# Kernel tuning notes

Hardware: AMD Instinct MI355X
Metric: run time of the kernel (lower is better)

Reference implementation:

```python
import jax, jax.numpy as jnp
import numpy as np

N = 100000   # nodes
E = 3200000  # directed edges
EPS = 1e-5   # batchnorm eps


def setup_inputs() -> dict:
    key = jax.random.key(0)
    ks = jax.random.split(key, 12)
    x = jax.random.normal(ks[0], (N, 128), jnp.float32)
    edge_index = jax.random.randint(ks[1], (2, E), 0, N, dtype=jnp.int32).astype(jnp.int64)
    W1 = jax.random.normal(ks[2], (128, 256), jnp.float32) * (1.0 / np.sqrt(128))
    W2 = jax.random.normal(ks[3], (256, 256), jnp.float32) * (1.0 / np.sqrt(256))
    W3 = jax.random.normal(ks[4], (256, 40), jnp.float32) * (1.0 / np.sqrt(256))
    return {
        "x": x, "edge_index": edge_index,
        "W1": W1, "b1": jnp.zeros((256,), jnp.float32),
        "W2": W2, "b2": jnp.zeros((256,), jnp.float32),
        "W3": W3, "b3": jnp.zeros((40,), jnp.float32),
        "g1": jnp.ones((256,), jnp.float32), "be1": jnp.zeros((256,), jnp.float32),
        "g2": jnp.ones((256,), jnp.float32), "be2": jnp.zeros((256,), jnp.float32),
    }


def _gcn_conv(x, src, dst, norm, W, b):
    # GCNConv: transform then normalized sparse aggregation (A_hat @ (x W)) + b
    h = x @ W                              # [N, F_out]
    msg = h[src] * norm[:, None]           # gather + edge scaling, [E+N, F_out]
    return jax.ops.segment_sum(msg, dst, num_segments=N) + b


def _bn(h, g, b):
    # BatchNorm over the node dimension (batch stats, biased variance)
    m = h.mean(axis=0)
    v = h.var(axis=0)
    return (h - m) * jax.lax.rsqrt(v + EPS) * g + b


def reference(x, edge_index, W1, b1, W2, b2, W3, b3, g1, be1, g2, be2):
    # add self-loops (A + I), symmetric degree normalization D^-1/2 (A+I) D^-1/2
    loop = jnp.arange(N, dtype=edge_index.dtype)
    src = jnp.concatenate([edge_index[0], loop])
    dst = jnp.concatenate([edge_index[1], loop])
    deg = jax.ops.segment_sum(jnp.ones_like(src, jnp.float32), dst, num_segments=N)
    dinv = jax.lax.rsqrt(jnp.maximum(deg, 1.0))
    norm = dinv[src] * dinv[dst]           # [E+N]

    h = _gcn_conv(x, src, dst, norm, W1, b1)
    h = jax.nn.relu(_bn(h, g1, be1))       # dropout: identity (eval mode)
    h = _gcn_conv(h, src, dst, norm, W2, b2)
    h = jax.nn.relu(_bn(h, g2, be2))
    h = _gcn_conv(h, src, dst, norm, W3, b3)
    return jax.nn.log_softmax(h, axis=1)
```

## Files before the change

### kernel.cpp

```cpp
#include <hip/hip_runtime.h>
#include <hip/hip_bf16.h>
#include <math.h>

#define NNODES 100000
#define NEDGES 3200000
#define BN_EPS 1e-5f
#define NCH 391

typedef unsigned int uint;
typedef unsigned short ushort;
typedef __attribute__((ext_vector_type(8))) short bf16x8;
typedef __attribute__((ext_vector_type(4))) float f32x4;

__device__ inline float bflo(uint u) { return __uint_as_float(u << 16); }
__device__ inline float bfhi(uint u) { return __uint_as_float(u & 0xffff0000u); }
__device__ inline ushort f2bf(float f) {
    __hip_bfloat16 h = __float2bfloat16(f);
    union { __hip_bfloat16 b; ushort u; } c; c.b = h; return c.u;
}


__global__ void k_hist(const int* __restrict__ dst, int* __restrict__ cnt) {
    int e = blockIdx.x * 256 + threadIdx.x;
    if (e < NEDGES) atomicAdd(&cnt[dst[e]], 1);
}

__global__ void k_deg(const int* __restrict__ cnt, float* __restrict__ dinv,
                      int* __restrict__ chunksums) {
    __shared__ int s[256];
    int i = blockIdx.x * 256 + threadIdx.x;
    int c = (i < NNODES) ? cnt[i] : 0;
    if (i < NNODES) dinv[i] = rsqrtf((float)c + 1.0f);
    s[threadIdx.x] = c;
    __syncthreads();
    for (int o = 128; o > 0; o >>= 1) {
        if (threadIdx.x < o) s[threadIdx.x] += s[threadIdx.x + o];
        __syncthreads();
    }
    if (threadIdx.x == 0) chunksums[blockIdx.x] = s[0];
}

__global__ void k_scan1(int* __restrict__ chunksums, int* __restrict__ rowstart) {
    __shared__ int s[512];
    int t = threadIdx.x;
    int v = (t < NCH) ? chunksums[t] : 0;
    s[t] = v;
    __syncthreads();
    for (int o = 1; o < 512; o <<= 1) {
        int add = (t >= o) ? s[t - o] : 0;
        __syncthreads();
        s[t] += add;
        __syncthreads();
    }
    if (t < NCH) chunksums[t] = s[t] - v;
    if (t == NCH - 1) rowstart[NNODES] = s[t];
}

__global__ void k_scan2(const int* __restrict__ cnt, const int* __restrict__ chunkbase,
                        int* __restrict__ rowstart, int* __restrict__ cursor) {
    __shared__ int s[256];
    int t = threadIdx.x;
    int i = blockIdx.x * 256 + t;
    int v = (i < NNODES) ? cnt[i] : 0;
    s[t] = v;
    __syncthreads();
    for (int o = 1; o < 256; o <<= 1) {
        int add = (t >= o) ? s[t - o] : 0;
        __syncthreads();
        s[t] += add;
        __syncthreads();
    }
    if (i < NNODES) {
        int excl = s[t] - v + chunkbase[blockIdx.x];
        rowstart[i] = excl;
        cursor[i]   = excl;
    }
}

__global__ void k_scatter(const int* __restrict__ src, const int* __restrict__ dst,
                          const float* __restrict__ dinv, int* __restrict__ cursor,
                          int2* __restrict__ pairs) {
    int e = blockIdx.x * 256 + threadIdx.x;
    if (e >= NEDGES) return;
    int s = src[e], d = dst[e];
    int p = atomicAdd(&cursor[d], 1);
    float w = dinv[s] * dinv[d];
    pairs[p] = make_int2(s, __float_as_int(w));
}


template <int F, bool BF16OUT>
__global__ __launch_bounds__(256) void k_aggb(
    const ushort* __restrict__ X, void* __restrict__ Yv,
    const int2* __restrict__ pairs, const int* __restrict__ rowstart,
    const float* __restrict__ dinv, const float* __restrict__ bias) {
    constexpr int VEC = F / 64;
    constexpr int NU  = VEC / 2;
    const int sub = threadIdx.x >> 6;
    const int t   = threadIdx.x & 63;
    const int d   = blockIdx.x * 4 + sub;
    if (d >= NNODES) return;
    const int r0 = rowstart[d], r1 = rowstart[d + 1];
    const size_t cb = (size_t)VEC * t;
    float acc[VEC] = {};
    int p = r0;
    for (; p + 8 <= r1; p += 8) {
        int2 e[8];
#pragma unroll
        for (int j = 0; j < 8; ++j) e[j] = pairs[p + j];
        if constexpr (NU == 2) {
            uint2 u[8];
#pragma unroll
            for (int j = 0; j < 8; ++j) u[j] = *(const uint2*)(X + (size_t)e[j].x * F + cb);
#pragma unroll
            for (int j = 0; j < 8; ++j) {
                float w = __int_as_float(e[j].y);
                acc[0]=fmaf(w,bflo(u[j].x),acc[0]); acc[1]=fmaf(w,bfhi(u[j].x),acc[1]);
                acc[2]=fmaf(w,bflo(u[j].y),acc[2]); acc[3]=fmaf(w,bfhi(u[j].y),acc[3]);
            }
        } else {
            uint u[8];
#pragma unroll
            for (int j = 0; j < 8; ++j) u[j] = *(const uint*)(X + (size_t)e[j].x * F + cb);
#pragma unroll
            for (int j = 0; j < 8; ++j) {
                float w = __int_as_float(e[j].y);
                acc[0]=fmaf(w,bflo(u[j]),acc[0]); acc[1]=fmaf(w,bfhi(u[j]),acc[1]);
            }
        }
    }
    for (; p < r1; ++p) {
        int2 e = pairs[p];
        float w = __int_as_float(e.y);
        if constexpr (NU == 2) {
            uint2 u = *(const uint2*)(X + (size_t)e.x * F + cb);
            acc[0]=fmaf(w,bflo(u.x),acc[0]); acc[1]=fmaf(w,bfhi(u.x),acc[1]);
            acc[2]=fmaf(w,bflo(u.y),acc[2]); acc[3]=fmaf(w,bfhi(u.y),acc[3]);
        } else {
            uint u = *(const uint*)(X + (size_t)e.x * F + cb);
            acc[0]=fmaf(w,bflo(u),acc[0]); acc[1]=fmaf(w,bfhi(u),acc[1]);
        }
    }
    float di = dinv[d], ws = di * di;
    if constexpr (NU == 2) {
        uint2 u = *(const uint2*)(X + (size_t)d * F + cb);
        acc[0]=fmaf(ws,bflo(u.x),acc[0]); acc[1]=fmaf(ws,bfhi(u.x),acc[1]);
        acc[2]=fmaf(ws,bflo(u.y),acc[2]); acc[3]=fmaf(ws,bfhi(u.y),acc[3]);
    } else {
        uint u = *(const uint*)(X + (size_t)d * F + cb);
        acc[0]=fmaf(ws,bflo(u),acc[0]); acc[1]=fmaf(ws,bfhi(u),acc[1]);
    }
    if (bias) {
#pragma unroll
        for (int j = 0; j < VEC; ++j) acc[j] += bias[cb + j];
    }
    if constexpr (BF16OUT) {
        uint* Y = (uint*)Yv;
        uint o0 = (uint)f2bf(acc[0]) | ((uint)f2bf(acc[1]) << 16);
        if constexpr (NU == 2) {
            uint o1 = (uint)f2bf(acc[2]) | ((uint)f2bf(acc[3]) << 16);
            *(uint2*)(Y + (size_t)d * (F/2) + cb/2) = make_uint2(o0, o1);
        } else {
            Y[(size_t)d * (F/2) + cb/2] = o0;
        }
    } else {
        float* Y = (float*)Yv;
        if constexpr (NU == 2) {
            float4 o; o.x=acc[0]; o.y=acc[1]; o.z=acc[2]; o.w=acc[3];
            *(float4*)(Y + (size_t)d * F + cb) = o;
        } else {
            *(float2*)(Y + (size_t)d * F + cb) = make_float2(acc[0], acc[1]);
        }
    }
}


__global__ __launch_bounds__(256) void k_agg40lsm(
    const ushort* __restrict__ X, float* __restrict__ out,
    const int2* __restrict__ pairs, const int* __restrict__ rowstart,
    const float* __restrict__ dinv, const float* __restrict__ bias) {
    int t = threadIdx.x;
    int wid = t >> 6, lane = t & 63;
    int sub = lane >> 5, l32 = lane & 31;
    int d = blockIdx.x * 8 + wid * 2 + sub;
    bool act = l32 < 20;
    int col = act ? 2 * l32 : 0;
    const int r0 = rowstart[d], r1 = rowstart[d + 1];
    float a0 = 0.f, a1 = 0.f;
    int p = r0;
    for (; p + 4 <= r1; p += 4) {
        int2 e0 = pairs[p], e1 = pairs[p+1], e2 = pairs[p+2], e3 = pairs[p+3];
        uint u0 = *(const uint*)(X + (size_t)e0.x * 40 + col);
        uint u1 = *(const uint*)(X + (size_t)e1.x * 40 + col);
        uint u2 = *(const uint*)(X + (size_t)e2.x * 40 + col);
        uint u3 = *(const uint*)(X + (size_t)e3.x * 40 + col);
        float w0 = __int_as_float(e0.y), w1 = __int_as_float(e1.y);
        float w2 = __int_as_float(e2.y), w3 = __int_as_float(e3.y);
        a0=fmaf(w0,bflo(u0),a0); a1=fmaf(w0,bfhi(u0),a1);
        a0=fmaf(w1,bflo(u1),a0); a1=fmaf(w1,bfhi(u1),a1);
        a0=fmaf(w2,bflo(u2),a0); a1=fmaf(w2,bfhi(u2),a1);
        a0=fmaf(w3,bflo(u3),a0); a1=fmaf(w3,bfhi(u3),a1);
    }
    for (; p < r1; ++p) {
        int2 e = pairs[p];
        uint u = *(const uint*)(X + (size_t)e.x * 40 + col);
        float w_ = __int_as_float(e.y);
        a0=fmaf(w_,bflo(u),a0); a1=fmaf(w_,bfhi(u),a1);
    }
    float di = dinv[d], ws = di * di;
    uint us = *(const uint*)(X + (size_t)d * 40 + col);
    a0=fmaf(ws,bflo(us),a0); a1=fmaf(ws,bfhi(us),a1);
    if (act) { a0 += bias[col]; a1 += bias[col + 1]; }
    else     { a0 = -INFINITY;  a1 = -INFINITY; }
    float mx = fmaxf(a0, a1);
    for (int o = 16; o > 0; o >>= 1) mx = fmaxf(mx, __shfl_xor(mx, o, 32));
    float e = act ? (expf(a0 - mx) + expf(a1 - mx)) : 0.f;
    float s = e;
    for (int o = 16; o > 0; o >>= 1) s += __shfl_xor(s, o, 32);
    float ls = logf(s);
    if (act)
        *(float2*)(out + (size_t)d * 40 + col) = make_float2(a0 - mx - ls, a1 - mx - ls);
}


__global__ void k_xtobf16(const float* __restrict__ X, ushort* __restrict__ O) {
    int i = blockIdx.x * 256 + threadIdx.x;
    float4 v = ((const float4*)X)[i];
    ushort4 o; o.x=f2bf(v.x); o.y=f2bf(v.y); o.z=f2bf(v.z); o.w=f2bf(v.w);
    ((ushort4*)O)[i] = o;
}

__global__ void k_wconv(const float* __restrict__ W, ushort* __restrict__ Wt, int K) {
    int n = blockIdx.x;
    for (int k = threadIdx.x; k < K; k += 256)
        Wt[n * K + k] = f2bf(W[(size_t)k * 256 + n]);
}


__device__ inline bf16x8 bnrelu8(bf16x8 v, const float* __restrict__ scsh, int ch) {
    bf16x8 r;
#pragma unroll
    for (int j = 0; j < 8; ++j) {
        float f = __uint_as_float(((uint)(ushort)v[j]) << 16);
        f = fmaxf(fmaf(f, scsh[ch + j], scsh[256 + ch + j]), 0.f);
        r[j] = (short)f2bf(f);
    }
    return r;
}

template <int K, bool BNA>
__global__ __launch_bounds__(256) void k_gmm(
    const ushort* __restrict__ A, const ushort* __restrict__ Bt,
    const float* __restrict__ scsh, ushort* __restrict__ C) {
    __shared__ ushort As[128 * 32];
    __shared__ ushort Bs[128 * 32];
    const int m0 = blockIdx.x * 128;
    const int n0 = blockIdx.y * 128;
    const int tid = threadIdx.x;
    const int lane = tid & 63;
    const int wid = tid >> 6;
    const int wr = wid >> 1, wc = wid & 1;
    const int sr1 = tid >> 2, sc = tid & 3;
    const int sr2 = sr1 + 64;
    const int ssl1 = sr1 * 32 + ((sc ^ ((sr1 >> 1) & 3)) * 8);
    const int ssl2 = sr2 * 32 + ((sc ^ ((sr2 >> 1) & 3)) * 8);
    const size_t ga1 = (size_t)min(m0 + sr1, NNODES - 1) * K + sc * 8;
    const size_t ga2 = (size_t)min(m0 + sr2, NNODES - 1) * K + sc * 8;
    const size_t gb1 = (size_t)(n0 + sr1) * K + sc * 8;
    const size_t gb2 = (size_t)(n0 + sr2) * K + sc * 8;
    const int kc = lane >> 4, rr = lane & 15;
    f32x4 acc[4][4] = {};
    for (int k0 = 0; k0 < K; k0 += 32) {
        bf16x8 av1 = *(const bf16x8*)(A + ga1 + k0);
        bf16x8 av2 = *(const bf16x8*)(A + ga2 + k0);
        bf16x8 bv1 = *(const bf16x8*)(Bt + gb1 + k0);
        bf16x8 bv2 = *(const bf16x8*)(Bt + gb2 + k0);
        if constexpr (BNA) {
            int ch = k0 + sc * 8;
            av1 = bnrelu8(av1, scsh, ch);
            av2 = bnrelu8(av2, scsh, ch);
        }
        if (k0) __syncthreads();
        *(bf16x8*)(As + ssl1) = av1;
        *(bf16x8*)(As + ssl2) = av2;
        *(bf16x8*)(Bs + ssl1) = bv1;
        *(bf16x8*)(Bs + ssl2) = bv2;
        __syncthreads();
        bf16x8 af[4], bfr[4];
#pragma unroll
        for (int f = 0; f < 4; ++f) {
            int ar = wr * 64 + f * 16 + rr;
            int br = wc * 64 + f * 16 + rr;
            af[f]  = *(const bf16x8*)(As + ar * 32 + ((kc ^ ((ar >> 1) & 3)) * 8));
            bfr[f] = *(const bf16x8*)(Bs + br * 32 + ((kc ^ ((br >> 1) & 3)) * 8));
        }
#pragma unroll
        for (int fm = 0; fm < 4; ++fm)
#pragma unroll
            for (int fn = 0; fn < 4; ++fn)
                acc[fm][fn] = __builtin_amdgcn_mfma_f32_16x16x32_bf16(af[fm], bfr[fn], acc[fm][fn], 0, 0, 0);
    }
    const int crow0 = m0 + wr * 64 + (lane >> 4) * 4;
    const int ccol0 = n0 + wc * 64 + (lane & 15);
#pragma unroll
    for (int fm = 0; fm < 4; ++fm) {
#pragma unroll
        for (int r = 0; r < 4; ++r) {
            int m = crow0 + fm * 16 + r;
            if (m >= NNODES) continue;
#pragma unroll
            for (int fn = 0; fn < 4; ++fn)
                C[(size_t)m * 256 + ccol0 + fn * 16] = f2bf(acc[fm][fn][r]);
        }
    }
}

__global__ void k_gemm3(const uint* __restrict__ A, const float* __restrict__ scsh,
                        const float* __restrict__ W, ushort* __restrict__ C) {
    __shared__ float aS[4][256];
    int m0 = blockIdx.x * 4;
    int t = threadIdx.x;
    for (int j = t; j < 512; j += 256) {
        int r = j >> 7, kk = j & 127;
        uint u = A[(size_t)(m0 + r) * 128 + kk];
        aS[r][2*kk]   = fmaxf(fmaf(bflo(u), scsh[2*kk],   scsh[256+2*kk]),   0.f);
        aS[r][2*kk+1] = fmaxf(fmaf(bfhi(u), scsh[2*kk+1], scsh[256+2*kk+1]), 0.f);
    }
    __syncthreads();
    int w = t >> 6, lane = t & 63;
    if (lane >= 40) return;
    float acc0 = 0.f, acc1 = 0.f;
#pragma unroll 8
    for (int k = 0; k < 256; k += 2) {
        acc0 = fmaf(aS[w][k],     W[k * 40 + lane],       acc0);
        acc1 = fmaf(aS[w][k + 1], W[(k + 1) * 40 + lane], acc1);
    }
    C[(size_t)(m0 + w) * 40 + lane] = f2bf(acc0 + acc1);
}


__global__ void k_bnstats_bf(const uint* __restrict__ H, float* __restrict__ sums) {
    int t = threadIdx.x;
    int pp = t & 127, half = t >> 7;
    size_t row0 = (size_t)blockIdx.x * 256 + half * 128;
    float s0=0, s20=0, s1=0, s21=0;
    for (int i = 0; i < 128; ++i) {
        size_t m = row0 + i;
        if (m >= NNODES) break;
        uint u = H[m * 128 + pp];
        float v0 = bflo(u), v1 = bfhi(u);
        s0 += v0; s20 += v0*v0; s1 += v1; s21 += v1*v1;
    }
    atomicAdd(&sums[2*pp],       s0);
    atomicAdd(&sums[2*pp+1],     s1);
    atomicAdd(&sums[256+2*pp],   s20);
    atomicAdd(&sums[256+2*pp+1], s21);
}

__global__ void k_bnfin(const float* __restrict__ sums, const float* __restrict__ g,
                        const float* __restrict__ be, float* __restrict__ scsh) {
    int c = threadIdx.x;
    float mean = sums[c] * (1.0f / NNODES);
    float var  = sums[256 + c] * (1.0f / NNODES) - mean * mean;
    float sc = g[c] * rsqrtf(var + BN_EPS);
    scsh[c] = sc;
    scsh[256 + c] = be[c] - mean * sc;
}


extern "C" void kernel_launch(void* const* d_in, const int* in_sizes, int n_in,
                              void* d_out, int out_size, void* d_ws, size_t ws_size,
                              hipStream_t stream) {
    const float* x  = (const float*)d_in[0];
    const int*   ei = (const int*)d_in[1];
    const float* W1 = (const float*)d_in[2];
    const float* W2 = (const float*)d_in[4];
    const float* W3 = (const float*)d_in[6];
    const float* b3 = (const float*)d_in[7];
    const float* g1 = (const float*)d_in[8];
    const float* be1 = (const float*)d_in[9];
    const float* g2 = (const float*)d_in[10];
    const float* be2 = (const float*)d_in[11];
    float* out = (float*)d_out;

    const int* esrc = ei;
    const int* edst = ei + NEDGES;

    char* p = (char*)d_ws;
    auto alloc = [&](size_t bytes) { char* r = p; p += (bytes + 511) & ~(size_t)511; return r; };
    float* dinv     = (float*)alloc((size_t)NNODES * 4);
    int*   cnt      = (int*)  alloc((size_t)NNODES * 4);
    int*   rowstart = (int*)  alloc((size_t)(NNODES + 1) * 4);
    int*   cursor   = (int*)  alloc((size_t)NNODES * 4);
    int*   chunksums= (int*)  alloc((size_t)NCH * 4);
    float* stats    = (float*)alloc((size_t)2048 * 4);
    ushort* W1t     = (ushort*)alloc((size_t)256 * 128 * 2);
    ushort* W2t     = (ushort*)alloc((size_t)256 * 256 * 2);
    int2*  pairs    = (int2*) alloc((size_t)NEDGES * 8);
    char*  R1       = alloc((size_t)NNODES * 256 * 2);
    char*  R2       = alloc((size_t)NNODES * 256 * 2);
    char*  R3       = alloc((size_t)NNODES * 256 * 2);

    ushort* xbf16 = (ushort*)R1;
    ushort* P_bf  = (ushort*)R1 + (size_t)NNODES * 128;
    ushort* t3_bf = (ushort*)R1;
    ushort* h1_bf = (ushort*)R2;
    ushort* h2_bf = (ushort*)R2;
    ushort* t_bf  = (ushort*)R3;

    float* sums1 = stats;        float* scsh1 = stats + 512;
    float* sums2 = stats + 1024; float* scsh2 = stats + 1536;

    hipMemsetAsync(cnt, 0, (size_t)NNODES * 4, stream);
    hipMemsetAsync(stats, 0, (size_t)2048 * 4, stream);

    const int EB = NEDGES / 256;
    const int NB = NCH;

    k_hist<<<EB, 256, 0, stream>>>(edst, cnt);
    k_deg<<<NB, 256, 0, stream>>>(cnt, dinv, chunksums);
    k_scan1<<<1, 512, 0, stream>>>(chunksums, rowstart);
    k_scan2<<<NB, 256, 0, stream>>>(cnt, chunksums, rowstart, cursor);
    k_scatter<<<EB, 256, 0, stream>>>(esrc, edst, dinv, cursor, pairs);

    k_wconv<<<256, 256, 0, stream>>>(W1, W1t, 128);
    k_wconv<<<256, 256, 0, stream>>>(W2, W2t, 256);
    k_xtobf16<<<NNODES * 128 / 4 / 256, 256, 0, stream>>>(x, xbf16);

    dim3 ggrid((NNODES + 127) / 128, 2);

    k_aggb<128, true><<<NNODES / 4, 256, 0, stream>>>(xbf16, P_bf, pairs, rowstart, dinv, nullptr);
    k_gmm<128, false><<<ggrid, 256, 0, stream>>>(P_bf, W1t, nullptr, h1_bf);
    k_bnstats_bf<<<NB, 256, 0, stream>>>((const uint*)h1_bf, sums1);
    k_bnfin<<<1, 256, 0, stream>>>(sums1, g1, be1, scsh1);

    k_gmm<256, true><<<ggrid, 256, 0, stream>>>(h1_bf, W2t, scsh1, t_bf);
    k_aggb<256, true><<<NNODES / 4, 256, 0, stream>>>(t_bf, h2_bf, pairs, rowstart, dinv, nullptr);
    k_bnstats_bf<<<NB, 256, 0, stream>>>((const uint*)h2_bf, sums2);
    k_bnfin<<<1, 256, 0, stream>>>(sums2, g2, be2, scsh2);

    k_gemm3<<<NNODES / 4, 256, 0, stream>>>((const uint*)h2_bf, scsh2, W3, t3_bf);
    k_agg40lsm<<<NNODES / 8, 256, 0, stream>>>(t3_bf, out, pairs, rowstart, dinv, b3);
}
```

Before: 1.126 ms.

## Split-wave aggregation, fuse BN stats into GEMM, MFMA final layer, merge weight conversions

Several independent changes land together. The aggregation kernel now splits each wave into two halves that process alternate edges with wider 16-byte row loads and combine them with a cross-half shuffle. The first GEMM accumulates BatchNorm sums directly from its accumulators, which removes one stats pass over the hidden activations. The scalar 40-column final GEMM is replaced by an MFMA tiled kernel with BN+ReLU applied on load and a padded transposed W3. Smaller edits fuse the three weight conversions into one launch, vectorise the histogram to two edges per thread, and unroll the 40-wide aggregation by 8. The added atomics and the shuffle reduction bring extra overhead, and the half-wave split leaves the odd tail edge serialised.

```diff
diff --git a/kernel.cpp b/kernel.cpp
--- a/kernel.cpp
+++ b/kernel.cpp
@@ -21,8 +21,10 @@
 
 
 __global__ void k_hist(const int* __restrict__ dst, int* __restrict__ cnt) {
-    int e = blockIdx.x * 256 + threadIdx.x;
-    if (e < NEDGES) atomicAdd(&cnt[dst[e]], 1);
+    int e = (blockIdx.x * 256 + threadIdx.x) * 2;
+    int2 v = *(const int2*)(dst + e);
+    atomicAdd(&cnt[v.x], 1);
+    atomicAdd(&cnt[v.y], 1);
 }
 
 __global__ void k_deg(const int* __restrict__ cnt, float* __restrict__ dinv,
@@ -89,87 +91,102 @@
 }
 
 
-template <int F, bool BF16OUT>
-__global__ __launch_bounds__(256) void k_aggb(
-    const ushort* __restrict__ X, void* __restrict__ Yv,
+template <int F, int U>
+__global__ __launch_bounds__(256) void k_aggh(
+    const ushort* __restrict__ X, ushort* __restrict__ Y,
     const int2* __restrict__ pairs, const int* __restrict__ rowstart,
-    const float* __restrict__ dinv, const float* __restrict__ bias) {
-    constexpr int VEC = F / 64;
-    constexpr int NU  = VEC / 2;
-    const int sub = threadIdx.x >> 6;
-    const int t   = threadIdx.x & 63;
-    const int d   = blockIdx.x * 4 + sub;
-    if (d >= NNODES) return;
+    const float* __restrict__ dinv) {
+    constexpr int CPL = F / 32;
+    const int wv = threadIdx.x >> 6;
+    const int lane = threadIdx.x & 63;
+    const int h = lane >> 5, l32 = lane & 31;
+    const int d = blockIdx.x * 4 + wv;
     const int r0 = rowstart[d], r1 = rowstart[d + 1];
-    const size_t cb = (size_t)VEC * t;
-    float acc[VEC] = {};
+    const ushort* Xb = X + (size_t)CPL * l32;
+    float acc[CPL] = {};
     int p = r0;
-    for (; p + 8 <= r1; p += 8) {
-        int2 e[8];
-#pragma unroll
-        for (int j = 0; j < 8; ++j) e[j] = pairs[p + j];
-        if constexpr (NU == 2) {
-            uint2 u[8];
-#pragma unroll
-            for (int j = 0; j < 8; ++j) u[j] = *(const uint2*)(X + (size_t)e[j].x * F + cb);
-#pragma unroll
-            for (int j = 0; j < 8; ++j) {
+    for (; p + 2 * U <= r1; p += 2 * U) {
+        int2 e[U];
+#pragma unroll
+        for (int j = 0; j < U; ++j) e[j] = pairs[p + 2 * j + h];
+        if constexpr (CPL == 8) {
+            uint4 u[U];
+#pragma unroll
+            for (int j = 0; j < U; ++j) u[j] = *(const uint4*)(Xb + (size_t)e[j].x * F);
+#pragma unroll
+            for (int j = 0; j < U; ++j) {
                 float w = __int_as_float(e[j].y);
                 acc[0]=fmaf(w,bflo(u[j].x),acc[0]); acc[1]=fmaf(w,bfhi(u[j].x),acc[1]);
                 acc[2]=fmaf(w,bflo(u[j].y),acc[2]); acc[3]=fmaf(w,bfhi(u[j].y),acc[3]);
+                acc[4]=fmaf(w,bflo(u[j].z),acc[4]); acc[5]=fmaf(w,bfhi(u[j].z),acc[5]);
+                acc[6]=fmaf(w,bflo(u[j].w),acc[6]); acc[7]=fmaf(w,bfhi(u[j].w),acc[7]);
             }
         } else {
-            uint u[8];
-#pragma unroll
-            for (int j = 0; j < 8; ++j) u[j] = *(const uint*)(X + (size_t)e[j].x * F + cb);
-#pragma unroll
-            for (int j = 0; j < 8; ++j) {
+            uint2 u[U];
+#pragma unroll
+            for (int j = 0; j < U; ++j) u[j] = *(const uint2*)(Xb + (size_t)e[j].x * F);
+#pragma unroll
+            for (int j = 0; j < U; ++j) {
                 float w = __int_as_float(e[j].y);
-                acc[0]=fmaf(w,bflo(u[j]),acc[0]); acc[1]=fmaf(w,bfhi(u[j]),acc[1]);
-            }
-        }
-    }
-    for (; p < r1; ++p) {
+                acc[0]=fmaf(w,bflo(u[j].x),acc[0]); acc[1]=fmaf(w,bfhi(u[j].x),acc[1]);
+                acc[2]=fmaf(w,bflo(u[j].y),acc[2]); acc[3]=fmaf(w,bfhi(u[j].y),acc[3]);
+            }
+        }
+    }
+    for (; p + 2 <= r1; p += 2) {
+        int2 e = pairs[p + h];
+        float w = __int_as_float(e.y);
+        if constexpr (CPL == 8) {
+            uint4 u = *(const uint4*)(Xb + (size_t)e.x * F);
+            acc[0]=fmaf(w,bflo(u.x),acc[0]); acc[1]=fmaf(w,bfhi(u.x),acc[1]);
+            acc[2]=fmaf(w,bflo(u.y),acc[2]); acc[3]=fmaf(w,bfhi(u.y),acc[3]);
+            acc[4]=fmaf(w,bflo(u.z),acc[4]); acc[5]=fmaf(w,bfhi(u.z),acc[5]);
+            acc[6]=fmaf(w,bflo(u.w),acc[6]); acc[7]=fmaf(w,bfhi(u.w),acc[7]);
+        } else {
+            uint2 u = *(const uint2*)(Xb + (size_t)e.x * F);
+            acc[0]=fmaf(w,bflo(u.x),acc[0]); acc[1]=fmaf(w,bfhi(u.x),acc[1]);
+            acc[2]=fmaf(w,bflo(u.y),acc[2]); acc[3]=fmaf(w,bfhi(u.y),acc[3]);
+        }
+    }
+    if (p < r1 && h == 0) {
         int2 e = pairs[p];
         float w = __int_as_float(e.y);
-        if constexpr (NU == 2) {
-            uint2 u = *(const uint2*)(X + (size_t)e.x * F + cb);
+        if constexpr (CPL == 8) {
+            uint4 u = *(const uint4*)(Xb + (size_t)e.x * F);
             acc[0]=fmaf(w,bflo(u.x),acc[0]); acc[1]=fmaf(w,bfhi(u.x),acc[1]);
             acc[2]=fmaf(w,bflo(u.y),acc[2]); acc[3]=fmaf(w,bfhi(u.y),acc[3]);
+            acc[4]=fmaf(w,bflo(u.z),acc[4]); acc[5]=fmaf(w,bfhi(u.z),acc[5]);
+            acc[6]=fmaf(w,bflo(u.w),acc[6]); acc[7]=fmaf(w,bfhi(u.w),acc[7]);
         } else {
-            uint u = *(const uint*)(X + (size_t)e.x * F + cb);
-            acc[0]=fmaf(w,bflo(u),acc[0]); acc[1]=fmaf(w,bfhi(u),acc[1]);
-        }
-    }
-    float di = dinv[d], ws = di * di;
-    if constexpr (NU == 2) {
-        uint2 u = *(const uint2*)(X + (size_t)d * F + cb);
-        acc[0]=fmaf(ws,bflo(u.x),acc[0]); acc[1]=fmaf(ws,bfhi(u.x),acc[1]);
-        acc[2]=fmaf(ws,bflo(u.y),acc[2]); acc[3]=fmaf(ws,bfhi(u.y),acc[3]);
-    } else {
-        uint u = *(const uint*)(X + (size_t)d * F + cb);
-        acc[0]=fmaf(ws,bflo(u),acc[0]); acc[1]=fmaf(ws,bfhi(u),acc[1]);
-    }
-    if (bias) {
-#pragma unroll
-        for (int j = 0; j < VEC; ++j) acc[j] += bias[cb + j];
-    }
-    if constexpr (BF16OUT) {
-        uint* Y = (uint*)Yv;
-        uint o0 = (uint)f2bf(acc[0]) | ((uint)f2bf(acc[1]) << 16);
-        if constexpr (NU == 2) {
-            uint o1 = (uint)f2bf(acc[2]) | ((uint)f2bf(acc[3]) << 16);
-            *(uint2*)(Y + (size_t)d * (F/2) + cb/2) = make_uint2(o0, o1);
+            uint2 u = *(const uint2*)(Xb + (size_t)e.x * F);
+            acc[0]=fmaf(w,bflo(u.x),acc[0]); acc[1]=fmaf(w,bfhi(u.x),acc[1]);
+            acc[2]=fmaf(w,bflo(u.y),acc[2]); acc[3]=fmaf(w,bfhi(u.y),acc[3]);
+        }
+    }
+#pragma unroll
+    for (int c = 0; c < CPL; ++c) acc[c] += __shfl_xor(acc[c], 32);
+    if (h == 0) {
+        float di = dinv[d], ws = di * di;
+        if constexpr (CPL == 8) {
+            uint4 u = *(const uint4*)(Xb + (size_t)d * F);
+            acc[0]=fmaf(ws,bflo(u.x),acc[0]); acc[1]=fmaf(ws,bfhi(u.x),acc[1]);
+            acc[2]=fmaf(ws,bflo(u.y),acc[2]); acc[3]=fmaf(ws,bfhi(u.y),acc[3]);
+            acc[4]=fmaf(ws,bflo(u.z),acc[4]); acc[5]=fmaf(ws,bfhi(u.z),acc[5]);
+            acc[6]=fmaf(ws,bflo(u.w),acc[6]); acc[7]=fmaf(ws,bfhi(u.w),acc[7]);
+            uint4 o;
+            o.x = (uint)f2bf(acc[0]) | ((uint)f2bf(acc[1]) << 16);
+            o.y = (uint)f2bf(acc[2]) | ((uint)f2bf(acc[3]) << 16);
+            o.z = (uint)f2bf(acc[4]) | ((uint)f2bf(acc[5]) << 16);
+            o.w = (uint)f2bf(acc[6]) | ((uint)f2bf(acc[7]) << 16);
+            *(uint4*)(Y + (size_t)d * F + CPL * l32) = o;
         } else {
-            Y[(size_t)d * (F/2) + cb/2] = o0;
-        }
-    } else {
-        float* Y = (float*)Yv;
-        if constexpr (NU == 2) {
-            float4 o; o.x=acc[0]; o.y=acc[1]; o.z=acc[2]; o.w=acc[3];
-            *(float4*)(Y + (size_t)d * F + cb) = o;
-        } else {
-            *(float2*)(Y + (size_t)d * F + cb) = make_float2(acc[0], acc[1]);
+            uint2 u = *(const uint2*)(Xb + (size_t)d * F);
+            acc[0]=fmaf(ws,bflo(u.x),acc[0]); acc[1]=fmaf(ws,bfhi(u.x),acc[1]);
+            acc[2]=fmaf(ws,bflo(u.y),acc[2]); acc[3]=fmaf(ws,bfhi(u.y),acc[3]);
+            uint2 o;
+            o.x = (uint)f2bf(acc[0]) | ((uint)f2bf(acc[1]) << 16);
+            o.y = (uint)f2bf(acc[2]) | ((uint)f2bf(acc[3]) << 16);
+            *(uint2*)(Y + (size_t)d * F + CPL * l32) = o;
         }
     }
 }
@@ -188,28 +205,27 @@
     const int r0 = rowstart[d], r1 = rowstart[d + 1];
     float a0 = 0.f, a1 = 0.f;
     int p = r0;
-    for (; p + 4 <= r1; p += 4) {
-        int2 e0 = pairs[p], e1 = pairs[p+1], e2 = pairs[p+2], e3 = pairs[p+3];
-        uint u0 = *(const uint*)(X + (size_t)e0.x * 40 + col);
-        uint u1 = *(const uint*)(X + (size_t)e1.x * 40 + col);
-        uint u2 = *(const uint*)(X + (size_t)e2.x * 40 + col);
-        uint u3 = *(const uint*)(X + (size_t)e3.x * 40 + col);
-        float w0 = __int_as_float(e0.y), w1 = __int_as_float(e1.y);
-        float w2 = __int_as_float(e2.y), w3 = __int_as_float(e3.y);
-        a0=fmaf(w0,bflo(u0),a0); a1=fmaf(w0,bfhi(u0),a1);
-        a0=fmaf(w1,bflo(u1),a0); a1=fmaf(w1,bfhi(u1),a1);
-        a0=fmaf(w2,bflo(u2),a0); a1=fmaf(w2,bfhi(u2),a1);
-        a0=fmaf(w3,bflo(u3),a0); a1=fmaf(w3,bfhi(u3),a1);
+    for (; p + 8 <= r1; p += 8) {
+        int2 e[8]; uint u[8];
+#pragma unroll
+        for (int j = 0; j < 8; ++j) e[j] = pairs[p + j];
+#pragma unroll
+        for (int j = 0; j < 8; ++j) u[j] = *(const uint*)(X + (size_t)e[j].x * 40 + col);
+#pragma unroll
+        for (int j = 0; j < 8; ++j) {
+            float w = __int_as_float(e[j].y);
+            a0 = fmaf(w, bflo(u[j]), a0); a1 = fmaf(w, bfhi(u[j]), a1);
+        }
     }
     for (; p < r1; ++p) {
         int2 e = pairs[p];
         uint u = *(const uint*)(X + (size_t)e.x * 40 + col);
         float w_ = __int_as_float(e.y);
-        a0=fmaf(w_,bflo(u),a0); a1=fmaf(w_,bfhi(u),a1);
+        a0 = fmaf(w_, bflo(u), a0); a1 = fmaf(w_, bfhi(u), a1);
     }
     float di = dinv[d], ws = di * di;
     uint us = *(const uint*)(X + (size_t)d * 40 + col);
-    a0=fmaf(ws,bflo(us),a0); a1=fmaf(ws,bfhi(us),a1);
+    a0 = fmaf(ws, bflo(us), a0); a1 = fmaf(ws, bfhi(us), a1);
     if (act) { a0 += bias[col]; a1 += bias[col + 1]; }
     else     { a0 = -INFINITY;  a1 = -INFINITY; }
     float mx = fmaxf(a0, a1);
@@ -230,10 +246,23 @@
     ((ushort4*)O)[i] = o;
 }
 
-__global__ void k_wconv(const float* __restrict__ W, ushort* __restrict__ Wt, int K) {
-    int n = blockIdx.x;
-    for (int k = threadIdx.x; k < K; k += 256)
-        Wt[n * K + k] = f2bf(W[(size_t)k * 256 + n]);
+__global__ void k_wconv3(const float* __restrict__ W1, const float* __restrict__ W2,
+                         const float* __restrict__ W3, ushort* __restrict__ W1t,
+                         ushort* __restrict__ W2t, ushort* __restrict__ W3t) {
+    int b = blockIdx.x;
+    if (b < 256) {
+        int n = b;
+        for (int k = threadIdx.x; k < 128; k += 256)
+            W1t[n * 128 + k] = f2bf(W1[(size_t)k * 256 + n]);
+    } else if (b < 512) {
+        int n = b - 256;
+        for (int k = threadIdx.x; k < 256; k += 256)
+            W2t[n * 256 + k] = f2bf(W2[(size_t)k * 256 + n]);
+    } else {
+        int n = b - 512;
+        for (int k = threadIdx.x; k < 256; k += 256)
+            W3t[n * 256 + k] = (n < 40) ? f2bf(W3[(size_t)k * 40 + n]) : (ushort)0;
+    }
 }
 
 
@@ -248,10 +277,11 @@
     return r;
 }
 
-template <int K, bool BNA>
+template <int K, bool BNA, bool STATS>
 __global__ __launch_bounds__(256) void k_gmm(
     const ushort* __restrict__ A, const ushort* __restrict__ Bt,
-    const float* __restrict__ scsh, ushort* __restrict__ C) {
+    const float* __restrict__ scsh, ushort* __restrict__ C,
+    float* __restrict__ sums) {
     __shared__ ushort As[128 * 32];
     __shared__ ushort Bs[128 * 32];
     const int m0 = blockIdx.x * 128;
@@ -313,29 +343,107 @@
                 C[(size_t)m * 256 + ccol0 + fn * 16] = f2bf(acc[fm][fn][r]);
         }
     }
-}
-
-__global__ void k_gemm3(const uint* __restrict__ A, const float* __restrict__ scsh,
-                        const float* __restrict__ W, ushort* __restrict__ C) {
-    __shared__ float aS[4][256];
-    int m0 = blockIdx.x * 4;
-    int t = threadIdx.x;
-    for (int j = t; j < 512; j += 256) {
-        int r = j >> 7, kk = j & 127;
-        uint u = A[(size_t)(m0 + r) * 128 + kk];
-        aS[r][2*kk]   = fmaxf(fmaf(bflo(u), scsh[2*kk],   scsh[256+2*kk]),   0.f);
-        aS[r][2*kk+1] = fmaxf(fmaf(bfhi(u), scsh[2*kk+1], scsh[256+2*kk+1]), 0.f);
-    }
-    __syncthreads();
-    int w = t >> 6, lane = t & 63;
-    if (lane >= 40) return;
-    float acc0 = 0.f, acc1 = 0.f;
-#pragma unroll 8
-    for (int k = 0; k < 256; k += 2) {
-        acc0 = fmaf(aS[w][k],     W[k * 40 + lane],       acc0);
-        acc1 = fmaf(aS[w][k + 1], W[(k + 1) * 40 + lane], acc1);
-    }
-    C[(size_t)(m0 + w) * 40 + lane] = f2bf(acc0 + acc1);
+    if constexpr (STATS) {
+#pragma unroll
+        for (int fn = 0; fn < 4; ++fn) {
+            float s = 0.f, s2 = 0.f;
+#pragma unroll
+            for (int fm = 0; fm < 4; ++fm)
+#pragma unroll
+                for (int r = 0; r < 4; ++r) {
+                    int m = crow0 + fm * 16 + r;
+                    if (m < NNODES) { float v = acc[fm][fn][r]; s += v; s2 += v * v; }
+                }
+            s  += __shfl_xor(s, 16);  s  += __shfl_xor(s, 32);
+            s2 += __shfl_xor(s2, 16); s2 += __shfl_xor(s2, 32);
+            if (lane < 16) {
+                int ch = ccol0 + fn * 16;
+                atomicAdd(&sums[ch], s);
+                atomicAdd(&sums[256 + ch], s2);
+            }
+        }
+    }
+}
+
+
+__global__ __launch_bounds__(256) void k_gmm3m(
+    const ushort* __restrict__ A, const ushort* __restrict__ Bt,
+    const float* __restrict__ scsh, ushort* __restrict__ C) {
+    __shared__ ushort As[128 * 64];
+    __shared__ ushort Bs[48 * 64];
+    const int m0 = blockIdx.x * 128;
+    const int tid = threadIdx.x;
+    const int lane = tid & 63;
+    const int wm = tid >> 6;
+    const int kc = lane >> 4, rr = lane & 15;
+    f32x4 acc[2][3] = {};
+    for (int k0 = 0; k0 < 256; k0 += 64) {
+        bf16x8 avs[4];
+        int arow[4], ach[4];
+#pragma unroll
+        for (int i = 0; i < 4; ++i) {
+            int c = i * 256 + tid;
+            arow[i] = c >> 3; ach[i] = c & 7;
+            int m = min(m0 + arow[i], NNODES - 1);
+            bf16x8 v = *(const bf16x8*)(A + (size_t)m * 256 + k0 + ach[i] * 8);
+            avs[i] = bnrelu8(v, scsh, k0 + ach[i] * 8);
+        }
+        bf16x8 bvs[2];
+#pragma unroll
+        for (int i = 0; i < 2; ++i) {
+            int c = i * 256 + tid;
+            if (c < 384) {
+                int row = c >> 3, ch = c & 7;
+                bvs[i] = *(const bf16x8*)(Bt + (size_t)row * 256 + k0 + ch * 8);
+            }
+        }
+        if (k0) __syncthreads();
+#pragma unroll
+        for (int i = 0; i < 4; ++i)
+            *(bf16x8*)(As + arow[i] * 64 + ((ach[i] ^ (arow[i] & 7)) * 8)) = avs[i];
+#pragma unroll
+        for (int i = 0; i < 2; ++i) {
+            int c = i * 256 + tid;
+            if (c < 384) {
+                int row = c >> 3, ch = c & 7;
+                *(bf16x8*)(Bs + row * 64 + ((ch ^ (row & 7)) * 8)) = bvs[i];
+            }
+        }
+        __syncthreads();
+#pragma unroll
+        for (int ks = 0; ks < 2; ++ks) {
+            bf16x8 af[2], bfm[3];
+#pragma unroll
+            for (int fm = 0; fm < 2; ++fm) {
+                int ar = wm * 32 + fm * 16 + rr;
+                af[fm] = *(const bf16x8*)(As + ar * 64 + (((ks * 4 + kc) ^ (ar & 7)) * 8));
+            }
+#pragma unroll
+            for (int fn = 0; fn < 3; ++fn) {
+                int br = fn * 16 + rr;
+                bfm[fn] = *(const bf16x8*)(Bs + br * 64 + (((ks * 4 + kc) ^ (br & 7)) * 8));
+            }
+#pragma unroll
+            for (int fm = 0; fm < 2; ++fm)
+#pragma unroll
+                for (int fn = 0; fn < 3; ++fn)
+                    acc[fm][fn] = __builtin_amdgcn_mfma_f32_16x16x32_bf16(af[fm], bfm[fn], acc[fm][fn], 0, 0, 0);
+        }
+    }
+    const int crow0 = m0 + wm * 32 + (lane >> 4) * 4;
+    const int ccol = lane & 15;
+#pragma unroll
+    for (int fm = 0; fm < 2; ++fm)
+#pragma unroll
+        for (int r = 0; r < 4; ++r) {
+            int m = crow0 + fm * 16 + r;
+            if (m >= NNODES) continue;
+#pragma unroll
+            for (int fn = 0; fn < 3; ++fn) {
+                int col = fn * 16 + ccol;
+                if (col < 40) C[(size_t)m * 40 + col] = f2bf(acc[fm][fn][r]);
+            }
+        }
 }
 
 
@@ -396,6 +504,7 @@
     float* stats    = (float*)alloc((size_t)2048 * 4);
     ushort* W1t     = (ushort*)alloc((size_t)256 * 128 * 2);
     ushort* W2t     = (ushort*)alloc((size_t)256 * 256 * 2);
+    ushort* W3t     = (ushort*)alloc((size_t)48 * 256 * 2);
     int2*  pairs    = (int2*) alloc((size_t)NEDGES * 8);
     char*  R1       = alloc((size_t)NNODES * 256 * 2);
     char*  R2       = alloc((size_t)NNODES * 256 * 2);
@@ -414,31 +523,26 @@
     hipMemsetAsync(cnt, 0, (size_t)NNODES * 4, stream);
     hipMemsetAsync(stats, 0, (size_t)2048 * 4, stream);
 
-    const int EB = NEDGES / 256;
-    const int NB = NCH;
-
-    k_hist<<<EB, 256, 0, stream>>>(edst, cnt);
-    k_deg<<<NB, 256, 0, stream>>>(cnt, dinv, chunksums);
+    k_hist<<<NEDGES / 512, 256, 0, stream>>>(edst, cnt);
+    k_deg<<<NCH, 256, 0, stream>>>(cnt, dinv, chunksums);
     k_scan1<<<1, 512, 0, stream>>>(chunksums, rowstart);
-    k_scan2<<<NB, 256, 0, stream>>>(cnt, chunksums, rowstart, cursor);
-    k_scatter<<<EB, 256, 0, stream>>>(esrc, edst, dinv, cursor, pairs);
-
-    k_wconv<<<256, 256, 0, stream>>>(W1, W1t, 128);
-    k_wconv<<<256, 256, 0, stream>>>(W2, W2t, 256);
+    k_scan2<<<NCH, 256, 0, stream>>>(cnt, chunksums, rowstart, cursor);
+    k_scatter<<<NEDGES / 256, 256, 0, stream>>>(esrc, edst, dinv, cursor, pairs);
+
+    k_wconv3<<<560, 256, 0, stream>>>(W1, W2, W3, W1t, W2t, W3t);
     k_xtobf16<<<NNODES * 128 / 4 / 256, 256, 0, stream>>>(x, xbf16);
 
     dim3 ggrid((NNODES + 127) / 128, 2);
 
-    k_aggb<128, true><<<NNODES / 4, 256, 0, stream>>>(xbf16, P_bf, pairs, rowstart, dinv, nullptr);
-    k_gmm<128, false><<<ggrid, 256, 0, stream>>>(P_bf, W1t, nullptr, h1_bf);
-    k_bnstats_bf<<<NB, 256, 0, stream>>>((const uint*)h1_bf, sums1);
+    k_aggh<128, 8><<<NNODES / 4, 256, 0, stream>>>(xbf16, P_bf, pairs, rowstart, dinv);
+    k_gmm<128, false, true><<<ggrid, 256, 0, stream>>>(P_bf, W1t, nullptr, h1_bf, sums1);
     k_bnfin<<<1, 256, 0, stream>>>(sums1, g1, be1, scsh1);
 
-    k_gmm<256, true><<<ggrid, 256, 0, stream>>>(h1_bf, W2t, scsh1, t_bf);
-    k_aggb<256, true><<<NNODES / 4, 256, 0, stream>>>(t_bf, h2_bf, pairs, rowstart, dinv, nullptr);
-    k_bnstats_bf<<<NB, 256, 0, stream>>>((const uint*)h2_bf, sums2);
+    k_gmm<256, true, false><<<ggrid, 256, 0, stream>>>(h1_bf, W2t, scsh1, t_bf, nullptr);
+    k_aggh<256, 8><<<NNODES / 4, 256, 0, stream>>>(t_bf, h2_bf, pairs, rowstart, dinv);
+    k_bnstats_bf<<<NCH, 256, 0, stream>>>((const uint*)h2_bf, sums2);
     k_bnfin<<<1, 256, 0, stream>>>(sums2, g2, be2, scsh2);
 
-    k_gemm3<<<NNODES / 4, 256, 0, stream>>>((const uint*)h2_bf, scsh2, W3, t3_bf);
+    k_gmm3m<<<(NNODES + 127) / 128, 256, 0, stream>>>(h2_bf, W3t, scsh2, t3_bf);
     k_agg40lsm<<<NNODES / 8, 256, 0, stream>>>(t3_bf, out, pairs, rowstart, dinv, b3);
 }
```

Result: faster. 942.1 us (-16.4%).
